# Optimization experiments

Measured on AMD Instinct MI355X. Metric: run time of the kernel, lower is better.

The kernel has to match this reference:

```python
import jax, jax.numpy as jnp
import numpy as np

N = 50176
E = 802816
G = 64
IN_DIM = 128
HID = 128
GLOB = 16
BN_EPS = 1e-5


def transformer_conv(x, src, dst, Wq, bq, Wk, bk, Wv, bv, Ws, bs):
    # PyG TransformerConv, heads=1, concat=True, root_weight=True, beta=False
    q = x @ Wq + bq          # [N, H]
    k = x @ Wk + bk          # [N, H]
    v = x @ Wv + bv          # [N, H]
    scale = 1.0 / jnp.sqrt(jnp.asarray(HID, x.dtype))
    logits = jnp.sum(q[dst] * k[src], axis=-1) * scale          # [E]
    m = jax.ops.segment_max(logits, dst, num_segments=N)        # [N]
    m = jnp.where(jnp.isfinite(m), m, 0.0)
    e = jnp.exp(logits - m[dst])                                # [E]
    s = jax.ops.segment_sum(e, dst, num_segments=N)             # [N]
    alpha = e / (s[dst] + 1e-16)                                # [E]
    agg = jax.ops.segment_sum(alpha[:, None] * v[src], dst, num_segments=N)
    return agg + x @ Ws + bs


def batch_norm(x, gamma, beta):
    mu = jnp.mean(x, axis=0)
    var = jnp.mean((x - mu) ** 2, axis=0)
    return gamma * (x - mu) / jnp.sqrt(var + BN_EPS) + beta


def setup_inputs() -> dict:
    key = jax.random.key(0)
    ks = jax.random.split(key, 32)
    d = {}
    d['x'] = jax.random.normal(ks[0], (N, IN_DIM), dtype=jnp.float32)
    d['edge_index'] = jax.random.randint(ks[1], (2, E), 0, N, dtype=jnp.int32)
    d['ptr'] = (jnp.arange(G + 1, dtype=jnp.int32) * (N // G))
    d['global_features'] = jax.random.normal(ks[2], (G, GLOB), dtype=jnp.float32)
    dims = [(IN_DIM, HID), (HID, HID)]
    ki = 3
    for l, (di, do) in enumerate(dims):
        for nm in ['Wq', 'Wk', 'Wv', 'Ws']:
            d[f'{nm}{l}'] = jax.random.normal(ks[ki], (di, do), dtype=jnp.float32) * 0.05; ki += 1
        for nm in ['bq', 'bk', 'bv', 'bs']:
            d[f'{nm}{l}'] = jnp.zeros((do,), dtype=jnp.float32)
        d[f'g{l}'] = jnp.ones((do,), dtype=jnp.float32)
        d[f'be{l}'] = jnp.zeros((do,), dtype=jnp.float32)
    d['fcW'] = jax.random.normal(ks[ki], (HID + GLOB, HID), dtype=jnp.float32) * 0.05; ki += 1
    d['fcb'] = jnp.zeros((HID,), dtype=jnp.float32)
    d['fc2W'] = jax.random.normal(ks[ki], (HID, 1), dtype=jnp.float32) * 0.05; ki += 1
    d['fc2b'] = jnp.zeros((1,), dtype=jnp.float32)
    return d


def reference(x, edge_index, ptr, global_features,
              Wq0, Wk0, Wv0, Ws0, bq0, bk0, bv0, bs0, g0, be0,
              Wq1, Wk1, Wv1, Ws1, bq1, bk1, bv1, bs1, g1, be1,
              fcW, fcb, fc2W, fc2b):
    src, dst = edge_index[0], edge_index[1]
    h = transformer_conv(x, src, dst, Wq0, bq0, Wk0, bk0, Wv0, bv0, Ws0, bs0)
    h = jax.nn.relu(batch_norm(h, g0, be0))
    h = transformer_conv(h, src, dst, Wq1, bq1, Wk1, bk1, Wv1, bv1, Ws1, bs1)
    h = jax.nn.relu(batch_norm(h, g1, be1))
    # broadcast per-graph global features to nodes using ptr boundaries
    graph_id = jnp.searchsorted(ptr, jnp.arange(N, dtype=ptr.dtype), side='right') - 1
    rep = global_features[graph_id]                              # [N, GLOB]
    h = jnp.concatenate([h, rep], axis=1)
    h = jax.nn.relu(h @ fcW + fcb)
    out = h @ fc2W + fc2b                                        # [N, 1]
    return out[:, 0]
```

## Files before the change

kernel.cpp:

```cpp
#include <hip/hip_runtime.h>
#include <math.h>

#define N_NODES 50176
#define N_EDGES 802816
#define HIDDEN  128
#define NGRAPH  64
#define BN_EPS  1e-5f
#define ATT_SCALE 0.08838834764831845f

typedef __attribute__((ext_vector_type(8))) short bf16x8;
typedef __attribute__((ext_vector_type(4))) float f32x4;

__device__ __forceinline__ float bflo(unsigned u) { return __uint_as_float(u << 16); }
__device__ __forceinline__ float bfhi(unsigned u) { return __uint_as_float(u & 0xffff0000u); }
__device__ __forceinline__ unsigned short f2bf(float f) {
    unsigned u = __float_as_uint(f);
    unsigned r = (u + 0x7fffu + ((u >> 16) & 1u)) >> 16;
    return (unsigned short)r;
}

__device__ __forceinline__ void bn_ab4(const float* __restrict__ S, const float* __restrict__ Q,
                                       const float* __restrict__ G, const float* __restrict__ BE,
                                       int c, float4& A, float4& B) {
    const float invN = 1.0f / (float)N_NODES;
    float4 s = *reinterpret_cast<const float4*>(&S[c]);
    float4 q = *reinterpret_cast<const float4*>(&Q[c]);
    float4 g = *reinterpret_cast<const float4*>(&G[c]);
    float4 e = *reinterpret_cast<const float4*>(&BE[c]);
    #define BNC(x) { float mu = s.x * invN; float va = q.x * invN - mu * mu; \
                     float iv = rsqrtf(va + BN_EPS); A.x = g.x * iv; B.x = e.x - mu * A.x; }
    BNC(x) BNC(y) BNC(z) BNC(w)
    #undef BNC
}

__global__ void hist_kernel(const int* __restrict__ dst, int* __restrict__ cnt) {
    int e = blockIdx.x * 256 + threadIdx.x;
    if (e < N_EDGES) atomicAdd(&cnt[dst[e]], 1);
}

__global__ void scan1_kernel(const int* __restrict__ cnt, int* __restrict__ row_ptr,
                             int* __restrict__ bsum) {
    __shared__ int sh[256];
    int t = threadIdx.x, b = blockIdx.x;
    int base = b * 1024 + t * 4;
    int v0 = cnt[base], v1 = cnt[base + 1], v2 = cnt[base + 2], v3 = cnt[base + 3];
    int tot = v0 + v1 + v2 + v3;
    sh[t] = tot; __syncthreads();
    for (int off = 1; off < 256; off <<= 1) {
        int x = (t >= off) ? sh[t - off] : 0;
        __syncthreads();
        sh[t] += x;
        __syncthreads();
    }
    int excl = sh[t] - tot;
    row_ptr[base]     = excl;
    row_ptr[base + 1] = excl + v0;
    row_ptr[base + 2] = excl + v0 + v1;
    row_ptr[base + 3] = excl + v0 + v1 + v2;
    if (t == 255) bsum[b] = sh[255];
}

__global__ void scan3_kernel(int* __restrict__ row_ptr, int* __restrict__ cur,
                             const int* __restrict__ bsum) {
    __shared__ int sh_off;
    int t = threadIdx.x, b = blockIdx.x;
    if (t < 64) {
        int v = (t < 49) ? bsum[t] : 0;
        int inc = v;
        #pragma unroll
        for (int o = 1; o < 64; o <<= 1) {
            int u = __shfl_up(inc, o, 64);
            if (t >= o) inc += u;
        }
        if (t == b) sh_off = inc - v;
        if (b == 48 && t == 48) row_ptr[N_NODES] = inc;
    }
    __syncthreads();
    int off = sh_off;
    int base = b * 1024 + t * 4;
    #pragma unroll
    for (int j = 0; j < 4; j++) {
        int v = row_ptr[base + j] + off;
        row_ptr[base + j] = v;
        cur[base + j] = v;
    }
}

__global__ void scatter_kernel(const int* __restrict__ src, const int* __restrict__ dst,
                               int* __restrict__ cur, int* __restrict__ edge_src) {
    int e = blockIdx.x * 256 + threadIdx.x;
    if (e < N_EDGES) {
        int d = dst[e];
        int slot = atomicAdd(&cur[d], 1);
        edge_src[slot] = src[e];
    }
}

__global__ void wprep_kernel(const float* __restrict__ Wq, const float* __restrict__ Wk,
                             const float* __restrict__ Wv, const float* __restrict__ Ws,
                             unsigned short* __restrict__ WT) {
    int mb = blockIdx.x;
    const float* W = (mb == 0) ? Wq : (mb == 1) ? Wk : (mb == 2) ? Wv : Ws;
    int t = threadIdx.x;
    int k = t >> 1, ch = t & 1;
    #pragma unroll 8
    for (int cc = 0; cc < 64; cc++) {
        int c = ch * 64 + cc;
        WT[((size_t)mb * 128 + c) * 128 + k] = f2bf(W[k * 128 + c]);
    }
}

__global__ __launch_bounds__(512, 4) void gemm_mfma(
    const float* __restrict__ in,
    const unsigned short* __restrict__ WT,
    const float* __restrict__ bq, const float* __restrict__ bk,
    const float* __restrict__ bv, const float* __restrict__ bs,
    unsigned short* __restrict__ qbf, unsigned short* __restrict__ kvb,
    float* __restrict__ hb,
    const float* __restrict__ bnS, const float* __restrict__ bnQ,
    const float* __restrict__ bnG, const float* __restrict__ bnBe)
{
    __shared__ unsigned char ldsA[16384];
    __shared__ unsigned char ldsKV[32768];
    int t = threadIdx.x;
    int n0 = blockIdx.x * 64;

    {
        int r = t >> 3, seg = t & 7;
        const float* srcp = in + (size_t)(n0 + r) * 128 + seg * 16;
        float4 f0 = *reinterpret_cast<const float4*>(srcp);
        float4 f1 = *reinterpret_cast<const float4*>(srcp + 4);
        float4 f2 = *reinterpret_cast<const float4*>(srcp + 8);
        float4 f3 = *reinterpret_cast<const float4*>(srcp + 12);
        if (bnS) {
            int kb = seg * 16;
            float4 a0, b0, a1, b1, a2, b2, a3, b3;
            bn_ab4(bnS, bnQ, bnG, bnBe, kb,      a0, b0);
            bn_ab4(bnS, bnQ, bnG, bnBe, kb + 4,  a1, b1);
            bn_ab4(bnS, bnQ, bnG, bnBe, kb + 8,  a2, b2);
            bn_ab4(bnS, bnQ, bnG, bnBe, kb + 12, a3, b3);
            f0.x = fmaxf(f0.x * a0.x + b0.x, 0.f); f0.y = fmaxf(f0.y * a0.y + b0.y, 0.f);
            f0.z = fmaxf(f0.z * a0.z + b0.z, 0.f); f0.w = fmaxf(f0.w * a0.w + b0.w, 0.f);
            f1.x = fmaxf(f1.x * a1.x + b1.x, 0.f); f1.y = fmaxf(f1.y * a1.y + b1.y, 0.f);
            f1.z = fmaxf(f1.z * a1.z + b1.z, 0.f); f1.w = fmaxf(f1.w * a1.w + b1.w, 0.f);
            f2.x = fmaxf(f2.x * a2.x + b2.x, 0.f); f2.y = fmaxf(f2.y * a2.y + b2.y, 0.f);
            f2.z = fmaxf(f2.z * a2.z + b2.z, 0.f); f2.w = fmaxf(f2.w * a2.w + b2.w, 0.f);
            f3.x = fmaxf(f3.x * a3.x + b3.x, 0.f); f3.y = fmaxf(f3.y * a3.y + b3.y, 0.f);
            f3.z = fmaxf(f3.z * a3.z + b3.z, 0.f); f3.w = fmaxf(f3.w * a3.w + b3.w, 0.f);
        }
        uint4 p0, p1;
        p0.x = (unsigned)f2bf(f0.x) | ((unsigned)f2bf(f0.y) << 16);
        p0.y = (unsigned)f2bf(f0.z) | ((unsigned)f2bf(f0.w) << 16);
        p0.z = (unsigned)f2bf(f1.x) | ((unsigned)f2bf(f1.y) << 16);
        p0.w = (unsigned)f2bf(f1.z) | ((unsigned)f2bf(f1.w) << 16);
        p1.x = (unsigned)f2bf(f2.x) | ((unsigned)f2bf(f2.y) << 16);
        p1.y = (unsigned)f2bf(f2.z) | ((unsigned)f2bf(f2.w) << 16);
        p1.z = (unsigned)f2bf(f3.x) | ((unsigned)f2bf(f3.y) << 16);
        p1.w = (unsigned)f2bf(f3.z) | ((unsigned)f2bf(f3.w) << 16);
        unsigned sw = (unsigned)((r & 7) << 4);
        *reinterpret_cast<uint4*>(&ldsA[r * 256 + (((unsigned)(seg * 32)) ^ sw)]) = p0;
        *reinterpret_cast<uint4*>(&ldsA[r * 256 + (((unsigned)(seg * 32 + 16)) ^ sw)]) = p1;
    }
    __syncthreads();

    int lane = t & 63, w = t >> 6;
    int m = w >> 1, half = w & 1;
    int lrow = lane & 15, lk = lane >> 4;

    f32x4 acc[4][4] = {};
    #pragma unroll
    for (int ks = 0; ks < 4; ks++) {
        bf16x8 bfr[4], af[4];
        #pragma unroll
        for (int j = 0; j < 4; j++) {
            int col = half * 64 + j * 16 + lrow;
            bfr[j] = *reinterpret_cast<const bf16x8*>(
                &WT[((size_t)m * 128 + col) * 128 + ks * 32 + lk * 8]);
        }
        #pragma unroll
        for (int i = 0; i < 4; i++) {
            unsigned row = (unsigned)(i * 16 + lrow);
            af[i] = *reinterpret_cast<const bf16x8*>(
                &ldsA[row * 256 + (((unsigned)(ks * 64 + lk * 16)) ^ ((row & 7) << 4))]);
        }
        #pragma unroll
        for (int i = 0; i < 4; i++)
            #pragma unroll
            for (int j = 0; j < 4; j++)
                acc[i][j] = __builtin_amdgcn_mfma_f32_16x16x32_bf16(af[i], bfr[j], acc[i][j], 0, 0, 0);
    }

    __syncthreads();

    const float* bias = (m == 0) ? bq : (m == 1) ? bk : (m == 2) ? bv : bs;
    if (m == 3) {
        #pragma unroll
        for (int j = 0; j < 4; j++) {
            int c = half * 64 + j * 16 + lrow;
            float bi = bias[c];
            #pragma unroll
            for (int i = 0; i < 4; i++)
                #pragma unroll
                for (int r4 = 0; r4 < 4; r4++) {
                    int row = n0 + i * 16 + lk * 4 + r4;
                    hb[(size_t)row * 128 + c] = acc[i][j][r4] + bi;
                }
        }
    } else if (m == 0) {
        #pragma unroll
        for (int j = 0; j < 4; j++) {
            int c = half * 64 + j * 16 + lrow;
            float bi = bias[c];
            #pragma unroll
            for (int i = 0; i < 4; i++)
                #pragma unroll
                for (int r4 = 0; r4 < 4; r4++) {
                    unsigned row = (unsigned)(i * 16 + lk * 4 + r4);
                    unsigned sw = ((row >> 2) & 3) << 5;
                    *reinterpret_cast<unsigned short*>(
                        &ldsA[row * 256 + (((unsigned)(2 * c)) ^ sw)]) =
                        f2bf(acc[i][j][r4] + bi);
                }
        }
    } else {
        unsigned vOff = (m == 1) ? 0u : 256u;
        #pragma unroll
        for (int j = 0; j < 4; j++) {
            int c = half * 64 + j * 16 + lrow;
            float bi = bias[c];
            unsigned bir = vOff + (unsigned)c * 2;
            #pragma unroll
            for (int i = 0; i < 4; i++)
                #pragma unroll
                for (int r4 = 0; r4 < 4; r4++) {
                    unsigned row = (unsigned)(i * 16 + lk * 4 + r4);
                    unsigned sw = ((row >> 2) & 3) << 5;
                    *reinterpret_cast<unsigned short*>(&ldsKV[row * 512 + (bir ^ sw)]) =
                        f2bf(acc[i][j][r4] + bi);
                }
        }
    }
    __syncthreads();

    {
        int r = t >> 3, seg = t & 7;
        unsigned sw = (((unsigned)r >> 2) & 3) << 5;
        char* qdst = (char*)(qbf + (size_t)(n0 + r) * 128) + seg * 32;
        uint4 v0 = *reinterpret_cast<const uint4*>(
            &ldsA[r * 256 + (((unsigned)(seg * 32)) ^ sw)]);
        uint4 v1 = *reinterpret_cast<const uint4*>(
            &ldsA[r * 256 + ((((unsigned)(seg * 32)) ^ sw) + 16)]);
        *reinterpret_cast<uint4*>(qdst) = v0;
        *reinterpret_cast<uint4*>(qdst + 16) = v1;
        char* dst = (char*)(kvb + (size_t)(n0 + r) * 256) + seg * 64;
        #pragma unroll
        for (int u = 0; u < 4; u++) {
            uint4 v = *reinterpret_cast<const uint4*>(
                &ldsKV[r * 512 + (((unsigned)(seg * 64 + u * 16)) ^ sw)]);
            *reinterpret_cast<uint4*>(dst + u * 16) = v;
        }
    }
}

__global__ __launch_bounds__(256) void agg_kernel(
    const unsigned short* __restrict__ qbf, const unsigned short* __restrict__ kvb,
    const int* __restrict__ row_ptr, const int* __restrict__ edge_src,
    float* __restrict__ hb)
{
    int wave = threadIdx.x >> 6, lane = threadIdx.x & 63;
    int n = blockIdx.x * 4 + wave;
    int quarter = lane >> 4, ql = lane & 15;

    uint4 qr = reinterpret_cast<const uint4*>(qbf + (size_t)n * 128)[ql];
    float q0 = bflo(qr.x), q1 = bfhi(qr.x), q2 = bflo(qr.y), q3 = bfhi(qr.y);
    float q4v = bflo(qr.z), q5 = bfhi(qr.z), q6 = bflo(qr.w), q7 = bfhi(qr.w);

    int s0 = row_ptr[n], s1 = row_ptr[n + 1];

    float acc0 = 0.f, acc1 = 0.f, acc2 = 0.f, acc3 = 0.f;
    float acc4 = 0.f, acc5 = 0.f, acc6 = 0.f, acc7 = 0.f;
    float ssum = 0.f;

    #define EDGE_ACC(kr, vr, act)                                          \
    {                                                                      \
        float part = q0 * bflo(kr.x) + q1 * bfhi(kr.x)                     \
                   + q2 * bflo(kr.y) + q3 * bfhi(kr.y)                     \
                   + q4v * bflo(kr.z) + q5 * bfhi(kr.z)                    \
                   + q6 * bflo(kr.w) + q7 * bfhi(kr.w);                    \
        part += __shfl_xor(part, 1, 64);                                   \
        part += __shfl_xor(part, 2, 64);                                   \
        part += __shfl_xor(part, 4, 64);                                   \
        part += __shfl_xor(part, 8, 64);                                   \
        float wgt = (act) ? __expf(part * ATT_SCALE) : 0.f;                \
        ssum += wgt;                                                       \
        acc0 += wgt * bflo(vr.x); acc1 += wgt * bfhi(vr.x);                \
        acc2 += wgt * bflo(vr.y); acc3 += wgt * bfhi(vr.y);                \
        acc4 += wgt * bflo(vr.z); acc5 += wgt * bfhi(vr.z);                \
        acc6 += wgt * bflo(vr.w); acc7 += wgt * bfhi(vr.w);                \
    }

    for (int j0 = s0; j0 < s1; j0 += 8) {
        int ja = j0 + quarter;
        int jb = ja + 4;
        bool aa = ja < s1, ab = jb < s1;
        int sa = aa ? edge_src[ja] : 0;
        int sb = ab ? edge_src[jb] : 0;
        const uint4* pa = reinterpret_cast<const uint4*>(kvb + (size_t)sa * 256);
        const uint4* pb = reinterpret_cast<const uint4*>(kvb + (size_t)sb * 256);
        uint4 kra = pa[ql], vra = pa[16 + ql];
        uint4 krb = pb[ql], vrb = pb[16 + ql];
        EDGE_ACC(kra, vra, aa)
        EDGE_ACC(krb, vrb, ab)
    }
    #undef EDGE_ACC

    #define XRED(x) { x += __shfl_xor(x, 16, 64); x += __shfl_xor(x, 32, 64); }
    XRED(acc0) XRED(acc1) XRED(acc2) XRED(acc3)
    XRED(acc4) XRED(acc5) XRED(acc6) XRED(acc7)
    XRED(ssum)
    #undef XRED

    if (quarter == 0) {
        float inv = 1.0f / (ssum + 1e-16f);
        float4 h0 = *reinterpret_cast<float4*>(&hb[(size_t)n * 128 + ql * 8]);
        float4 h1 = *reinterpret_cast<float4*>(&hb[(size_t)n * 128 + ql * 8 + 4]);
        h0.x += acc0 * inv; h0.y += acc1 * inv; h0.z += acc2 * inv; h0.w += acc3 * inv;
        h1.x += acc4 * inv; h1.y += acc5 * inv; h1.z += acc6 * inv; h1.w += acc7 * inv;
        *reinterpret_cast<float4*>(&hb[(size_t)n * 128 + ql * 8]) = h0;
        *reinterpret_cast<float4*>(&hb[(size_t)n * 128 + ql * 8 + 4]) = h1;
    }
}

__global__ __launch_bounds__(256) void bn_stats(const float* __restrict__ h,
                                                float* __restrict__ sums,
                                                float* __restrict__ sqs) {
    int t = threadIdx.x;
    float4 s4 = make_float4(0.f, 0.f, 0.f, 0.f);
    float4 q4 = make_float4(0.f, 0.f, 0.f, 0.f);
    const int stride = 784 * 256;
    for (int i = blockIdx.x * 256 + t; i < N_NODES * 32; i += stride) {
        float4 v = reinterpret_cast<const float4*>(h)[i];
        s4.x += v.x; s4.y += v.y; s4.z += v.z; s4.w += v.w;
        q4.x += v.x * v.x; q4.y += v.y * v.y; q4.z += v.z * v.z; q4.w += v.w * v.w;
    }
    __shared__ float sh_s[1024], sh_q[1024];
    sh_s[t * 4 + 0] = s4.x; sh_s[t * 4 + 1] = s4.y; sh_s[t * 4 + 2] = s4.z; sh_s[t * 4 + 3] = s4.w;
    sh_q[t * 4 + 0] = q4.x; sh_q[t * 4 + 1] = q4.y; sh_q[t * 4 + 2] = q4.z; sh_q[t * 4 + 3] = q4.w;
    __syncthreads();
    if (t < 128) {
        float ss = 0.f, qq = 0.f;
        #pragma unroll
        for (int r = 0; r < 8; r++) { ss += sh_s[t + 128 * r]; qq += sh_q[t + 128 * r]; }
        atomicAdd(&sums[t], ss);
        atomicAdd(&sqs[t], qq);
    }
}

__global__ __launch_bounds__(256) void fc_kernel(
    const float* __restrict__ h2,
    const float* __restrict__ bnS, const float* __restrict__ bnQ,
    const float* __restrict__ bnG, const float* __restrict__ bnBe,
    const int* __restrict__ ptr, const float* __restrict__ gf,
    const float* __restrict__ fcW, const float* __restrict__ fcb,
    const float* __restrict__ fc2W, const float* __restrict__ fc2b,
    float* __restrict__ out)
{
    __shared__ float hc[8][144];
    __shared__ float red[8][128];
    int t = threadIdx.x;
    int nb = blockIdx.x * 8;

    {
        int node_l = t >> 5, li = t & 31;
        int n = nb + node_l;
        float4 v = *reinterpret_cast<const float4*>(&h2[(size_t)n * 128 + li * 4]);
        float4 av, bv;
        bn_ab4(bnS, bnQ, bnG, bnBe, li * 4, av, bv);
        hc[node_l][li * 4 + 0] = fmaxf(v.x * av.x + bv.x, 0.f);
        hc[node_l][li * 4 + 1] = fmaxf(v.y * av.y + bv.y, 0.f);
        hc[node_l][li * 4 + 2] = fmaxf(v.z * av.z + bv.z, 0.f);
        hc[node_l][li * 4 + 3] = fmaxf(v.w * av.w + bv.w, 0.f);
        if (li < 16) {
            int lo = 0, hi = NGRAPH;
            while (lo < hi) {
                int mid = (lo + hi + 1) >> 1;
                if (ptr[mid] <= n) lo = mid; else hi = mid - 1;
            }
            hc[node_l][128 + li] = gf[lo * 16 + li];
        }
    }
    __syncthreads();

    {
        int half = t >> 7, o = t & 127;
        float fb = fcb[o];
        float acc0 = fb, acc1 = fb, acc2 = fb, acc3 = fb;
        const float* h0 = hc[half * 4 + 0];
        const float* h1 = hc[half * 4 + 1];
        const float* h2c = hc[half * 4 + 2];
        const float* h3 = hc[half * 4 + 3];
        #pragma unroll 16
        for (int i = 0; i < 144; i++) {
            float w = fcW[i * 128 + o];
            acc0 += h0[i] * w;
            acc1 += h1[i] * w;
            acc2 += h2c[i] * w;
            acc3 += h3[i] * w;
        }
        float w2 = fc2W[o];
        red[half * 4 + 0][o] = fmaxf(acc0, 0.f) * w2;
        red[half * 4 + 1][o] = fmaxf(acc1, 0.f) * w2;
        red[half * 4 + 2][o] = fmaxf(acc2, 0.f) * w2;
        red[half * 4 + 3][o] = fmaxf(acc3, 0.f) * w2;
    }
    __syncthreads();

    {
        int node_l = t >> 5, li = t & 31;
        float s = red[node_l][li] + red[node_l][li + 32]
                + red[node_l][li + 64] + red[node_l][li + 96];
        s += __shfl_xor(s, 1, 64);
        s += __shfl_xor(s, 2, 64);
        s += __shfl_xor(s, 4, 64);
        s += __shfl_xor(s, 8, 64);
        s += __shfl_xor(s, 16, 64);
        if (li == 0) out[nb + node_l] = s + fc2b[0];
    }
}

extern "C" void kernel_launch(void* const* d_in, const int* in_sizes, int n_in,
                              void* d_out, int out_size, void* d_ws, size_t ws_size,
                              hipStream_t stream)
{
    const float* x   = (const float*)d_in[0];
    const int*   ei  = (const int*)d_in[1];
    const int*   ptr = (const int*)d_in[2];
    const float* gf  = (const float*)d_in[3];
    const float* Wq0 = (const float*)d_in[4];
    const float* Wk0 = (const float*)d_in[5];
    const float* Wv0 = (const float*)d_in[6];
    const float* Ws0 = (const float*)d_in[7];
    const float* bq0 = (const float*)d_in[8];
    const float* bk0 = (const float*)d_in[9];
    const float* bv0 = (const float*)d_in[10];
    const float* bs0 = (const float*)d_in[11];
    const float* g0  = (const float*)d_in[12];
    const float* be0 = (const float*)d_in[13];
    const float* Wq1 = (const float*)d_in[14];
    const float* Wk1 = (const float*)d_in[15];
    const float* Wv1 = (const float*)d_in[16];
    const float* Ws1 = (const float*)d_in[17];
    const float* bq1 = (const float*)d_in[18];
    const float* bk1 = (const float*)d_in[19];
    const float* bv1 = (const float*)d_in[20];
    const float* bs1 = (const float*)d_in[21];
    const float* g1  = (const float*)d_in[22];
    const float* be1 = (const float*)d_in[23];
    const float* fcW = (const float*)d_in[24];
    const float* fcb = (const float*)d_in[25];
    const float* fc2W= (const float*)d_in[26];
    const float* fc2b= (const float*)d_in[27];
    float* out = (float*)d_out;

    const int* src_p = ei;
    const int* dst_p = ei + N_EDGES;

    char* w = (char*)d_ws;
    const size_t NM = (size_t)N_NODES * 128 * sizeof(float);
    unsigned short* qbf = (unsigned short*)w;  w += (size_t)N_NODES * 128 * sizeof(unsigned short);
    unsigned short* kvb = (unsigned short*)w;  w += (size_t)N_NODES * 256 * sizeof(unsigned short);
    float* h1 = (float*)w;                     w += NM;
    float* h2 = (float*)w;                     w += NM;
    float* stats = (float*)w;                  w += 512 * sizeof(float);
    float* sums0 = stats;
    float* sqs0  = stats + 128;
    float* sums1 = stats + 256;
    float* sqs1  = stats + 384;
    unsigned short* WT0 = (unsigned short*)w;  w += (size_t)512 * 128 * sizeof(unsigned short);
    unsigned short* WT1 = (unsigned short*)w;  w += (size_t)512 * 128 * sizeof(unsigned short);
    int* cnt     = (int*)w;                    w += (size_t)N_NODES * sizeof(int);
    int* row_ptr = (int*)w;                    w += (size_t)(N_NODES + 1) * sizeof(int);
    int* cur     = (int*)w;                    w += (size_t)N_NODES * sizeof(int);
    int* edge_src= (int*)w;                    w += (size_t)N_EDGES * sizeof(int);
    int* bsum    = (int*)w;                    w += 64 * sizeof(int);

    hipMemsetAsync(cnt, 0, (size_t)N_NODES * sizeof(int), stream);
    hipMemsetAsync(stats, 0, 512 * sizeof(float), stream);

    wprep_kernel<<<4, 256, 0, stream>>>(Wq0, Wk0, Wv0, Ws0, WT0);
    wprep_kernel<<<4, 256, 0, stream>>>(Wq1, Wk1, Wv1, Ws1, WT1);

    hist_kernel<<<3136, 256, 0, stream>>>(dst_p, cnt);
    scan1_kernel<<<49, 256, 0, stream>>>(cnt, row_ptr, bsum);
    scan3_kernel<<<49, 256, 0, stream>>>(row_ptr, cur, bsum);
    scatter_kernel<<<3136, 256, 0, stream>>>(src_p, dst_p, cur, edge_src);

    gemm_mfma<<<784, 512, 0, stream>>>(x, WT0,
        bq0, bk0, bv0, bs0, qbf, kvb, h1, nullptr, nullptr, nullptr, nullptr);
    agg_kernel<<<12544, 256, 0, stream>>>(qbf, kvb, row_ptr, edge_src, h1);
    bn_stats<<<784, 256, 0, stream>>>(h1, sums0, sqs0);

    gemm_mfma<<<784, 512, 0, stream>>>(h1, WT1,
        bq1, bk1, bv1, bs1, qbf, kvb, h2, sums0, sqs0, g0, be0);
    agg_kernel<<<12544, 256, 0, stream>>>(qbf, kvb, row_ptr, edge_src, h2);
    bn_stats<<<784, 256, 0, stream>>>(h2, sums1, sqs1);

    fc_kernel<<<6272, 256, 0, stream>>>(h2, sums1, sqs1, g1, be1, ptr, gf,
        fcW, fcb, fc2W, fc2b, out);
}
```

Baseline: 509.5 us.

## Move final FC layer onto bf16 MFMA and unroll edge aggregation loop

Replaces the scalar fp32 FC head with an MFMA-based kernel. Each block of 64 nodes stages BN+ReLU outputs and the per-graph features as bf16 in LDS, multiplies them against a pre-transposed, zero-padded bf16 fcW, and fuses the fc2 reduction into the epilogue. A small prep kernel builds the transposed weight. The aggregation loop also processes 4 edges per quarter-wave per iteration instead of 2, so more gathers are in flight. The cost is lower precision in the FC layer and more register pressure in the aggregation kernel.

Result: slower. 539.4 us (+5.9%).

```diff
diff --git a/kernel.cpp b/kernel.cpp
--- a/kernel.cpp
+++ b/kernel.cpp
@@ -108,6 +108,12 @@
         int c = ch * 64 + cc;
         WT[((size_t)mb * 128 + c) * 128 + k] = f2bf(W[k * 128 + c]);
     }
+}
+
+__global__ void fcprep_kernel(const float* __restrict__ fcW, unsigned short* __restrict__ fcWT) {
+    int c = threadIdx.x;
+    for (int k = 0; k < 160; k++)
+        fcWT[(size_t)c * 160 + k] = (k < 144) ? f2bf(fcW[k * 128 + c]) : (unsigned short)0;
 }
 
 __global__ __launch_bounds__(512, 4) void gemm_mfma(
@@ -299,18 +305,26 @@
         acc6 += wgt * bflo(vr.w); acc7 += wgt * bfhi(vr.w);                \
     }
 
-    for (int j0 = s0; j0 < s1; j0 += 8) {
+    for (int j0 = s0; j0 < s1; j0 += 16) {
         int ja = j0 + quarter;
-        int jb = ja + 4;
-        bool aa = ja < s1, ab = jb < s1;
+        int jb = ja + 4, jc = ja + 8, jd = ja + 12;
+        bool aa = ja < s1, ab = jb < s1, ac = jc < s1, ad = jd < s1;
         int sa = aa ? edge_src[ja] : 0;
         int sb = ab ? edge_src[jb] : 0;
+        int sc = ac ? edge_src[jc] : 0;
+        int sd = ad ? edge_src[jd] : 0;
         const uint4* pa = reinterpret_cast<const uint4*>(kvb + (size_t)sa * 256);
         const uint4* pb = reinterpret_cast<const uint4*>(kvb + (size_t)sb * 256);
+        const uint4* pc = reinterpret_cast<const uint4*>(kvb + (size_t)sc * 256);
+        const uint4* pd = reinterpret_cast<const uint4*>(kvb + (size_t)sd * 256);
         uint4 kra = pa[ql], vra = pa[16 + ql];
         uint4 krb = pb[ql], vrb = pb[16 + ql];
+        uint4 krc = pc[ql], vrc = pc[16 + ql];
+        uint4 krd = pd[ql], vrd = pd[16 + ql];
         EDGE_ACC(kra, vra, aa)
         EDGE_ACC(krb, vrb, ab)
+        EDGE_ACC(krc, vrc, ac)
+        EDGE_ACC(krd, vrd, ad)
     }
     #undef EDGE_ACC
 
@@ -356,76 +370,148 @@
     }
 }
 
-__global__ __launch_bounds__(256) void fc_kernel(
+__global__ __launch_bounds__(256) void fc_mfma(
     const float* __restrict__ h2,
     const float* __restrict__ bnS, const float* __restrict__ bnQ,
     const float* __restrict__ bnG, const float* __restrict__ bnBe,
     const int* __restrict__ ptr, const float* __restrict__ gf,
-    const float* __restrict__ fcW, const float* __restrict__ fcb,
+    const unsigned short* __restrict__ fcWT, const float* __restrict__ fcb,
     const float* __restrict__ fc2W, const float* __restrict__ fc2b,
     float* __restrict__ out)
 {
-    __shared__ float hc[8][144];
-    __shared__ float red[8][128];
+    __shared__ unsigned char ldsA[64 * 336];
+    __shared__ float bnAs[128], bnBs[128];
+    __shared__ float red[64][4];
     int t = threadIdx.x;
-    int nb = blockIdx.x * 8;
+    int n0 = blockIdx.x * 64;
+
+    if (t < 128) {
+        const float invN = 1.0f / (float)N_NODES;
+        float mu = bnS[t] * invN;
+        float va = bnQ[t] * invN - mu * mu;
+        float iv = rsqrtf(va + BN_EPS);
+        float a = bnG[t] * iv;
+        bnAs[t] = a;
+        bnBs[t] = bnBe[t] - mu * a;
+    }
+    __syncthreads();
 
     {
-        int node_l = t >> 5, li = t & 31;
-        int n = nb + node_l;
-        float4 v = *reinterpret_cast<const float4*>(&h2[(size_t)n * 128 + li * 4]);
-        float4 av, bv;
-        bn_ab4(bnS, bnQ, bnG, bnBe, li * 4, av, bv);
-        hc[node_l][li * 4 + 0] = fmaxf(v.x * av.x + bv.x, 0.f);
-        hc[node_l][li * 4 + 1] = fmaxf(v.y * av.y + bv.y, 0.f);
-        hc[node_l][li * 4 + 2] = fmaxf(v.z * av.z + bv.z, 0.f);
-        hc[node_l][li * 4 + 3] = fmaxf(v.w * av.w + bv.w, 0.f);
-        if (li < 16) {
+        int r = t & 63, part = t >> 6;
+        int n = n0 + r;
+        unsigned rb = (unsigned)r * 336;
+        if (part < 3) {
+            int c0 = part * 32;
+            const float* hp = h2 + (size_t)n * 128 + c0;
+            #pragma unroll
+            for (int u = 0; u < 4; u++) {
+                int cc = c0 + u * 8;
+                float4 fa = *reinterpret_cast<const float4*>(hp + u * 8);
+                float4 fbv = *reinterpret_cast<const float4*>(hp + u * 8 + 4);
+                uint4 pk;
+                float e0 = fmaxf(fa.x * bnAs[cc + 0] + bnBs[cc + 0], 0.f);
+                float e1 = fmaxf(fa.y * bnAs[cc + 1] + bnBs[cc + 1], 0.f);
+                float e2 = fmaxf(fa.z * bnAs[cc + 2] + bnBs[cc + 2], 0.f);
+                float e3 = fmaxf(fa.w * bnAs[cc + 3] + bnBs[cc + 3], 0.f);
+                float e4 = fmaxf(fbv.x * bnAs[cc + 4] + bnBs[cc + 4], 0.f);
+                float e5 = fmaxf(fbv.y * bnAs[cc + 5] + bnBs[cc + 5], 0.f);
+                float e6 = fmaxf(fbv.z * bnAs[cc + 6] + bnBs[cc + 6], 0.f);
+                float e7 = fmaxf(fbv.w * bnAs[cc + 7] + bnBs[cc + 7], 0.f);
+                pk.x = (unsigned)f2bf(e0) | ((unsigned)f2bf(e1) << 16);
+                pk.y = (unsigned)f2bf(e2) | ((unsigned)f2bf(e3) << 16);
+                pk.z = (unsigned)f2bf(e4) | ((unsigned)f2bf(e5) << 16);
+                pk.w = (unsigned)f2bf(e6) | ((unsigned)f2bf(e7) << 16);
+                *reinterpret_cast<uint4*>(&ldsA[rb + (unsigned)cc * 2]) = pk;
+            }
+        } else {
+            int c0 = 96;
+            const float* hp = h2 + (size_t)n * 128 + c0;
+            #pragma unroll
+            for (int u = 0; u < 4; u++) {
+                int cc = c0 + u * 8;
+                float4 fa = *reinterpret_cast<const float4*>(hp + u * 8);
+                float4 fbv = *reinterpret_cast<const float4*>(hp + u * 8 + 4);
+                uint4 pk;
+                float e0 = fmaxf(fa.x * bnAs[cc + 0] + bnBs[cc + 0], 0.f);
+                float e1 = fmaxf(fa.y * bnAs[cc + 1] + bnBs[cc + 1], 0.f);
+                float e2 = fmaxf(fa.z * bnAs[cc + 2] + bnBs[cc + 2], 0.f);
+                float e3 = fmaxf(fa.w * bnAs[cc + 3] + bnBs[cc + 3], 0.f);
+                float e4 = fmaxf(fbv.x * bnAs[cc + 4] + bnBs[cc + 4], 0.f);
+                float e5 = fmaxf(fbv.y * bnAs[cc + 5] + bnBs[cc + 5], 0.f);
+                float e6 = fmaxf(fbv.z * bnAs[cc + 6] + bnBs[cc + 6], 0.f);
+                float e7 = fmaxf(fbv.w * bnAs[cc + 7] + bnBs[cc + 7], 0.f);
+                pk.x = (unsigned)f2bf(e0) | ((unsigned)f2bf(e1) << 16);
+                pk.y = (unsigned)f2bf(e2) | ((unsigned)f2bf(e3) << 16);
+                pk.z = (unsigned)f2bf(e4) | ((unsigned)f2bf(e5) << 16);
+                pk.w = (unsigned)f2bf(e6) | ((unsigned)f2bf(e7) << 16);
+                *reinterpret_cast<uint4*>(&ldsA[rb + (unsigned)cc * 2]) = pk;
+            }
             int lo = 0, hi = NGRAPH;
             while (lo < hi) {
                 int mid = (lo + hi + 1) >> 1;
                 if (ptr[mid] <= n) lo = mid; else hi = mid - 1;
             }
-            hc[node_l][128 + li] = gf[lo * 16 + li];
-        }
-    }
-    __syncthreads();
-
-    {
-        int half = t >> 7, o = t & 127;
-        float fb = fcb[o];
-        float acc0 = fb, acc1 = fb, acc2 = fb, acc3 = fb;
-        const float* h0 = hc[half * 4 + 0];
-        const float* h1 = hc[half * 4 + 1];
-        const float* h2c = hc[half * 4 + 2];
-        const float* h3 = hc[half * 4 + 3];
-        #pragma unroll 16
-        for (int i = 0; i < 144; i++) {
-            float w = fcW[i * 128 + o];
-            acc0 += h0[i] * w;
-            acc1 += h1[i] * w;
-            acc2 += h2c[i] * w;
-            acc3 += h3[i] * w;
-        }
-        float w2 = fc2W[o];
-        red[half * 4 + 0][o] = fmaxf(acc0, 0.f) * w2;
-        red[half * 4 + 1][o] = fmaxf(acc1, 0.f) * w2;
-        red[half * 4 + 2][o] = fmaxf(acc2, 0.f) * w2;
-        red[half * 4 + 3][o] = fmaxf(acc3, 0.f) * w2;
-    }
-    __syncthreads();
-
-    {
-        int node_l = t >> 5, li = t & 31;
-        float s = red[node_l][li] + red[node_l][li + 32]
-                + red[node_l][li + 64] + red[node_l][li + 96];
-        s += __shfl_xor(s, 1, 64);
-        s += __shfl_xor(s, 2, 64);
-        s += __shfl_xor(s, 4, 64);
-        s += __shfl_xor(s, 8, 64);
-        s += __shfl_xor(s, 16, 64);
-        if (li == 0) out[nb + node_l] = s + fc2b[0];
-    }
+            const float* gp = gf + lo * 16;
+            #pragma unroll
+            for (int u = 0; u < 2; u++) {
+                float4 fa = *reinterpret_cast<const float4*>(gp + u * 8);
+                float4 fbv = *reinterpret_cast<const float4*>(gp + u * 8 + 4);
+                uint4 pk;
+                pk.x = (unsigned)f2bf(fa.x) | ((unsigned)f2bf(fa.y) << 16);
+                pk.y = (unsigned)f2bf(fa.z) | ((unsigned)f2bf(fa.w) << 16);
+                pk.z = (unsigned)f2bf(fbv.x) | ((unsigned)f2bf(fbv.y) << 16);
+                pk.w = (unsigned)f2bf(fbv.z) | ((unsigned)f2bf(fbv.w) << 16);
+                *reinterpret_cast<uint4*>(&ldsA[rb + 256 + u * 16]) = pk;
+            }
+            uint4 z = make_uint4(0, 0, 0, 0);
+            *reinterpret_cast<uint4*>(&ldsA[rb + 288]) = z;
+            *reinterpret_cast<uint4*>(&ldsA[rb + 304]) = z;
+            *reinterpret_cast<uint4*>(&ldsA[rb + 320]) = z;
+        }
+    }
+    __syncthreads();
+
+    int lane = t & 63, w = t >> 6;
+    int lrow = lane & 15, lk = lane >> 4;
+    int colA = w * 32 + lrow;
+    int colB = w * 32 + 16 + lrow;
+
+    f32x4 acc[4][2] = {};
+    #pragma unroll
+    for (int ks = 0; ks < 5; ks++) {
+        bf16x8 bfr[2], af[4];
+        bfr[0] = *reinterpret_cast<const bf16x8*>(&fcWT[(size_t)colA * 160 + ks * 32 + lk * 8]);
+        bfr[1] = *reinterpret_cast<const bf16x8*>(&fcWT[(size_t)colB * 160 + ks * 32 + lk * 8]);
+        #pragma unroll
+        for (int i = 0; i < 4; i++) {
+            unsigned row = (unsigned)(i * 16 + lrow);
+            af[i] = *reinterpret_cast<const bf16x8*>(&ldsA[row * 336 + ks * 64 + lk * 16]);
+        }
+        #pragma unroll
+        for (int i = 0; i < 4; i++) {
+            acc[i][0] = __builtin_amdgcn_mfma_f32_16x16x32_bf16(af[i], bfr[0], acc[i][0], 0, 0, 0);
+            acc[i][1] = __builtin_amdgcn_mfma_f32_16x16x32_bf16(af[i], bfr[1], acc[i][1], 0, 0, 0);
+        }
+    }
+
+    float fb0 = fcb[colA], fb1 = fcb[colB];
+    float w20 = fc2W[colA], w21 = fc2W[colB];
+    #pragma unroll
+    for (int i = 0; i < 4; i++) {
+        #pragma unroll
+        for (int r4 = 0; r4 < 4; r4++) {
+            float s = fmaxf(acc[i][0][r4] + fb0, 0.f) * w20
+                    + fmaxf(acc[i][1][r4] + fb1, 0.f) * w21;
+            s += __shfl_xor(s, 1, 64);
+            s += __shfl_xor(s, 2, 64);
+            s += __shfl_xor(s, 4, 64);
+            s += __shfl_xor(s, 8, 64);
+            if (lrow == 0) red[i * 16 + lk * 4 + r4][w] = s;
+        }
+    }
+    __syncthreads();
+    if (t < 64)
+        out[n0 + t] = red[t][0] + red[t][1] + red[t][2] + red[t][3] + fc2b[0];
 }
 
 extern "C" void kernel_launch(void* const* d_in, const int* in_sizes, int n_in,
@@ -478,6 +564,7 @@
     float* sqs1  = stats + 384;
     unsigned short* WT0 = (unsigned short*)w;  w += (size_t)512 * 128 * sizeof(unsigned short);
     unsigned short* WT1 = (unsigned short*)w;  w += (size_t)512 * 128 * sizeof(unsigned short);
+    unsigned short* fcWT = (unsigned short*)w; w += (size_t)128 * 160 * sizeof(unsigned short);
     int* cnt     = (int*)w;                    w += (size_t)N_NODES * sizeof(int);
     int* row_ptr = (int*)w;                    w += (size_t)(N_NODES + 1) * sizeof(int);
     int* cur     = (int*)w;                    w += (size_t)N_NODES * sizeof(int);
@@ -489,6 +576,7 @@
 
     wprep_kernel<<<4, 256, 0, stream>>>(Wq0, Wk0, Wv0, Ws0, WT0);
     wprep_kernel<<<4, 256, 0, stream>>>(Wq1, Wk1, Wv1, Ws1, WT1);
+    fcprep_kernel<<<1, 128, 0, stream>>>(fcW, fcWT);
 
     hist_kernel<<<3136, 256, 0, stream>>>(dst_p, cnt);
     scan1_kernel<<<49, 256, 0, stream>>>(cnt, row_ptr, bsum);
@@ -505,6 +593,6 @@
     agg_kernel<<<12544, 256, 0, stream>>>(qbf, kvb, row_ptr, edge_src, h2);
     bn_stats<<<784, 256, 0, stream>>>(h2, sums1, sqs1);
 
-    fc_kernel<<<6272, 256, 0, stream>>>(h2, sums1, sqs1, g1, be1, ptr, gf,
-        fcW, fcb, fc2W, fc2b, out);
-}
+    fc_mfma<<<784, 256, 0, stream>>>(h2, sums1, sqs1, g1, be1, ptr, gf,
+        fcWT, fcb, fc2W, fc2b, out);
+}
```
